# Optimization experiments

Measured on AMD Instinct MI355X. Metric: run time of the kernel, lower is better.

Reference implementation:

```python
import jax, jax.numpy as jnp
import numpy as np


def _conv1x1(x, w, b):
    # x: [B,C,H,W], w: [O,C], b: [O] -> [B,O,H,W]
    return jnp.einsum('bchw,oc->bohw', x, w) + b[None, :, None, None]


def setup_inputs() -> dict:
    key = jax.random.key(0)
    ks = jax.random.split(key, 5)
    B, C, H, W = 4, 256, 64, 64
    C2 = C // 2
    scale = 0.02  # keep attention logits in a sane range
    return {
        'x': jax.random.normal(ks[0], (B, C, H, W), dtype=jnp.float32),
        'w_theta': jax.random.normal(ks[1], (C2, C), dtype=jnp.float32) * scale,
        'b_theta': jnp.zeros((C2,), dtype=jnp.float32),
        'w_phi': jax.random.normal(ks[2], (C2, C), dtype=jnp.float32) * scale,
        'b_phi': jnp.zeros((C2,), dtype=jnp.float32),
        'w_g': jax.random.normal(ks[3], (C2, C), dtype=jnp.float32) * scale,
        'b_g': jnp.zeros((C2,), dtype=jnp.float32),
        'w_out': jax.random.normal(ks[4], (C, C2), dtype=jnp.float32) * scale,
        'b_out': jnp.zeros((C,), dtype=jnp.float32),
    }


def reference(x, w_theta, b_theta, w_phi, b_phi, w_g, b_g, w_out, b_out):
    B, C, H, W = x.shape
    C2 = C // 2
    N = H * W
    theta = _conv1x1(x, w_theta, b_theta).reshape(B, C2, N)  # [B,C2,N]
    phi = _conv1x1(x, w_phi, b_phi).reshape(B, C2, N)        # [B,C2,N]
    g = _conv1x1(x, w_g, b_g).reshape(B, C2, N)              # [B,C2,N]
    # non-local attention: scores[b,m,n] = theta[b,:,m] . phi[b,:,n]
    scores = jnp.einsum('bcm,bcn->bmn', theta, phi)          # [B,N,N]
    attn = jax.nn.softmax(scores, axis=-1)                   # [B,N,N]
    # output = g @ attn^T : out[b,c,m] = sum_n g[b,c,n] * attn[b,m,n]
    out = jnp.einsum('bcn,bmn->bcm', g, attn)                # [B,C2,N]
    out = out.reshape(B, C2, H, W)
    return x + _conv1x1(out, w_out, b_out)
```

## Files before the change

kernel.cpp:

```cpp
#include <hip/hip_runtime.h>
#include <hip/hip_bf16.h>

#define B_  4
#define C_  256
#define C2_ 128
#define N_  4096
#define LOG2E 1.4426950408889634f

typedef unsigned short u16;
typedef __attribute__((ext_vector_type(8))) short bf16x8;
typedef __attribute__((ext_vector_type(4))) float f32x4;

static __device__ __forceinline__ u16 f2bf(float f) {
    return __builtin_bit_cast(u16, __float2bfloat16(f));
}
static __device__ __forceinline__ float bf2f(u16 u) {
    return __bfloat162float(__builtin_bit_cast(__hip_bfloat16, u));
}

__global__ __launch_bounds__(256) void prepw_kernel(
    const float* __restrict__ wt, const float* __restrict__ wp,
    const float* __restrict__ wg, const float* __restrict__ wo,
    u16* __restrict__ Wb) {
    int i = (blockIdx.x * 256 + threadIdx.x) * 4;
    int mat = i >> 15, off = i & 32767;
    const float* src = mat == 0 ? wt : (mat == 1 ? wp : (mat == 2 ? wg : wo));
    float4 v = *(const float4*)(src + off);
    ushort4 o = { f2bf(v.x), f2bf(v.y), f2bf(v.z), f2bf(v.w) };
    *(ushort4*)(Wb + i) = o;
}

__global__ __launch_bounds__(256) void projx_kernel(
    const float* __restrict__ x, const u16* __restrict__ Wb,
    const float* __restrict__ b_theta, const float* __restrict__ b_phi,
    const float* __restrict__ b_g,
    u16* __restrict__ Q, u16* __restrict__ K, u16* __restrict__ V) {
    __shared__ __align__(16) union {
        u16 XTs[32][264];
        u16 Vt[128][40];
    } sm;
    int bid = blockIdx.x;
    int b   = bid / (N_ / 32);
    int n0  = (bid % (N_ / 32)) * 32;
    int tid = threadIdx.x;
    int wave = tid >> 6, lane = tid & 63, quad = lane >> 4, l16 = lane & 15;
    int mgrp = wave >> 1, chalf = wave & 1;

#pragma unroll
    for (int it = 0; it < 4; ++it) {
        int idx = it * 256 + tid;
        int q = idx & 7, p = idx >> 3;
        const float* r0 = x + ((size_t)b * C_ + 2 * p) * N_ + n0 + 4 * q;
        float4 v0 = *(const float4*)r0;
        float4 v1 = *(const float4*)(r0 + N_);
        const float* f0 = (const float*)&v0;
        const float* f1 = (const float*)&v1;
#pragma unroll
        for (int j = 0; j < 4; ++j) {
            unsigned pk = (unsigned)f2bf(f0[j]) | ((unsigned)f2bf(f1[j]) << 16);
            *(unsigned*)&sm.XTs[4 * q + j][2 * p] = pk;
        }
    }
    __syncthreads();

    bf16x8 af[8];
#pragma unroll
    for (int ks = 0; ks < 8; ++ks)
        af[ks] = *(const bf16x8*)&sm.XTs[mgrp * 16 + l16][ks * 32 + quad * 8];
    __syncthreads();

    const float* biases[3] = { b_theta, b_phi, b_g };
#pragma unroll
    for (int mat = 0; mat < 3; ++mat) {
        const u16* wm = Wb + (size_t)mat * C2_ * C_;
        const float* bias = biases[mat];
        f32x4 acc[4];
#pragma unroll
        for (int i = 0; i < 4; ++i) acc[i] = (f32x4){0.f, 0.f, 0.f, 0.f};
#pragma unroll
        for (int ct = 0; ct < 4; ++ct) {
            int ce = chalf * 4 + ct;
            const u16* wr = wm + (size_t)(ce * 16 + l16) * C_ + quad * 8;
#pragma unroll
            for (int ks = 0; ks < 8; ++ks) {
                bf16x8 bf = *(const bf16x8*)(wr + ks * 32);
                acc[ct] = __builtin_amdgcn_mfma_f32_16x16x32_bf16(af[ks], bf, acc[ct], 0, 0, 0);
            }
        }
        if (mat < 2) {
            u16* dst = mat == 0 ? Q : K;
            float sc = mat == 0 ? LOG2E : 1.0f;
#pragma unroll
            for (int ct = 0; ct < 4; ++ct) {
                int c2 = (chalf * 4 + ct) * 16 + l16;
                float bb = bias[c2];
#pragma unroll
                for (int r = 0; r < 4; ++r) {
                    int n = n0 + mgrp * 16 + quad * 4 + r;
                    dst[((size_t)b * N_ + n) * C2_ + c2] = f2bf((acc[ct][r] + bb) * sc);
                }
            }
        } else {
#pragma unroll
            for (int ct = 0; ct < 4; ++ct) {
                int c2 = (chalf * 4 + ct) * 16 + l16;
                float bb = bias[c2];
#pragma unroll
                for (int r = 0; r < 4; ++r)
                    sm.Vt[c2][mgrp * 16 + quad * 4 + r] = f2bf(acc[ct][r] + bb);
            }
        }
    }
    __syncthreads();
    {
        int row = tid >> 1, col16 = (tid & 1) * 16;
        uint4 a0 = *(const uint4*)&sm.Vt[row][col16];
        uint4 a1 = *(const uint4*)&sm.Vt[row][col16 + 8];
        u16* vp = V + ((size_t)b * C2_ + row) * N_ + n0 + col16;
        *(uint4*)vp = a0;
        *(uint4*)(vp + 8) = a1;
    }
}

__global__ __launch_bounds__(256, 2) void attn_kernel(
    const u16* __restrict__ Q, const u16* __restrict__ K,
    const u16* __restrict__ V, u16* __restrict__ AO,
    u16* __restrict__ Opb, float* __restrict__ lsum, int nsplit) {
    const int BM = 128, BN = 64, D = C2_;
    const int per = B_ * (N_ / BM);
    int s    = blockIdx.x / per;
    int r0   = blockIdx.x % per;
    int b    = r0 / (N_ / BM);
    int m0   = (r0 % (N_ / BM)) * BM;
    int tid  = threadIdx.x;
    int wave = tid >> 6, lane = tid & 63, quad = (lane >> 4) & 3, l16 = lane & 15;

    __shared__ __align__(16) u16 Ks[BN][D + 8];
    __shared__ __align__(16) u16 Vs[D][BN + 8];
    __shared__ __align__(16) u16 Psb[4][32][BN + 8];
    u16* Ps = &Psb[wave][0][0];

    bf16x8 qf[2][4];
#pragma unroll
    for (int ms = 0; ms < 2; ++ms) {
        const u16* qp = Q + ((size_t)b * N_ + m0 + wave * 32 + ms * 16 + l16) * D;
#pragma unroll
        for (int kk = 0; kk < 4; ++kk)
            qf[ms][kk] = *(const bf16x8*)(qp + kk * 32 + quad * 8);
    }

    float l_r[2][4] = {{0.f, 0.f, 0.f, 0.f}, {0.f, 0.f, 0.f, 0.f}};
    f32x4 o_acc[2][8];
#pragma unroll
    for (int ms = 0; ms < 2; ++ms)
#pragma unroll
        for (int i = 0; i < 8; ++i) o_acc[ms][i] = (f32x4){0.f, 0.f, 0.f, 0.f};

    const int tiles = N_ / BN;
    const int base = tiles / nsplit, rem = tiles % nsplit;
    const int t0 = s * base + (s < rem ? s : rem);
    const int cnt = base + (s < rem ? 1 : 0);
    const int nt0 = t0 * BN, nt1 = (t0 + cnt) * BN;

    for (int nt = nt0; nt < nt1; nt += BN) {
        const u16* kp = K + ((size_t)b * N_ + nt) * D;
#pragma unroll
        for (int it = 0; it < 4; ++it) {
            int idx = it * 256 + tid;
            int row = idx >> 4, col = (idx & 15) * 8;
            *(uint4*)&Ks[row][col] = *(const uint4*)(kp + row * D + col);
        }
#pragma unroll
        for (int it = 0; it < 4; ++it) {
            int idx = it * 256 + tid;
            int row = idx >> 3, col = (idx & 7) * 8;
            *(uint4*)&Vs[row][col] =
                *(const uint4*)(V + ((size_t)b * C2_ + row) * N_ + nt + col);
        }
        __syncthreads();

        f32x4 sc[2][4];
#pragma unroll
        for (int nn = 0; nn < 4; ++nn) {
            f32x4 a0 = (f32x4){0.f, 0.f, 0.f, 0.f};
            f32x4 a1 = (f32x4){0.f, 0.f, 0.f, 0.f};
#pragma unroll
            for (int kk = 0; kk < 4; ++kk) {
                bf16x8 kf = *(const bf16x8*)&Ks[nn * 16 + l16][kk * 32 + quad * 8];
                a0 = __builtin_amdgcn_mfma_f32_16x16x32_bf16(qf[0][kk], kf, a0, 0, 0, 0);
                a1 = __builtin_amdgcn_mfma_f32_16x16x32_bf16(qf[1][kk], kf, a1, 0, 0, 0);
            }
            sc[0][nn] = a0;
            sc[1][nn] = a1;
        }

#pragma unroll
        for (int ms = 0; ms < 2; ++ms)
#pragma unroll
            for (int nn = 0; nn < 4; ++nn)
#pragma unroll
                for (int r = 0; r < 4; ++r) {
                    float p = __builtin_amdgcn_exp2f(sc[ms][nn][r]);
                    l_r[ms][r] += p;
                    Ps[(ms * 16 + quad * 4 + r) * (BN + 8) + nn * 16 + l16] = f2bf(p);
                }

#pragma unroll
        for (int ks = 0; ks < 2; ++ks) {
            bf16x8 pf0 = *(const bf16x8*)&Ps[(l16) * (BN + 8) + ks * 32 + quad * 8];
            bf16x8 pf1 = *(const bf16x8*)&Ps[(16 + l16) * (BN + 8) + ks * 32 + quad * 8];
#pragma unroll
            for (int cs = 0; cs < 8; ++cs) {
                bf16x8 vf = *(const bf16x8*)&Vs[cs * 16 + l16][ks * 32 + quad * 8];
                o_acc[0][cs] = __builtin_amdgcn_mfma_f32_16x16x32_bf16(pf0, vf, o_acc[0][cs], 0, 0, 0);
                o_acc[1][cs] = __builtin_amdgcn_mfma_f32_16x16x32_bf16(pf1, vf, o_acc[1][cs], 0, 0, 0);
            }
        }
        __syncthreads();
    }

#pragma unroll
    for (int ms = 0; ms < 2; ++ms)
#pragma unroll
        for (int r = 0; r < 4; ++r) {
            l_r[ms][r] += __shfl_xor(l_r[ms][r], 1);
            l_r[ms][r] += __shfl_xor(l_r[ms][r], 2);
            l_r[ms][r] += __shfl_xor(l_r[ms][r], 4);
            l_r[ms][r] += __shfl_xor(l_r[ms][r], 8);
        }

    if (Opb) {
#pragma unroll
        for (int ms = 0; ms < 2; ++ms) {
#pragma unroll
            for (int cs = 0; cs < 8; ++cs)
#pragma unroll
                for (int r = 0; r < 4; ++r) {
                    size_t row = (size_t)s * (B_ * N_) + (size_t)b * N_ +
                                 m0 + wave * 32 + ms * 16 + quad * 4 + r;
                    Opb[row * C2_ + cs * 16 + l16] = f2bf(o_acc[ms][cs][r]);
                }
            if (l16 == 0)
#pragma unroll
                for (int r = 0; r < 4; ++r) {
                    size_t row = (size_t)s * (B_ * N_) + (size_t)b * N_ +
                                 m0 + wave * 32 + ms * 16 + quad * 4 + r;
                    lsum[row] = l_r[ms][r];
                }
        }
    } else {
#pragma unroll
        for (int ms = 0; ms < 2; ++ms)
#pragma unroll
            for (int cs = 0; cs < 8; ++cs)
#pragma unroll
                for (int r = 0; r < 4; ++r) {
                    float v = o_acc[ms][cs][r] / l_r[ms][r];
                    AO[((size_t)b * N_ + m0 + wave * 32 + ms * 16 + quad * 4 + r) * C2_ +
                       cs * 16 + l16] = f2bf(v);
                }
    }
}

__global__ __launch_bounds__(256) void outproj_kernel(
    const float* __restrict__ x, const u16* __restrict__ Opb,
    const float* __restrict__ lsum, const u16* __restrict__ AO,
    const u16* __restrict__ Wob, const float* __restrict__ b_out,
    float* __restrict__ y, int nsplit) {
    __shared__ __align__(16) u16 As[64][C2_ + 8];
    __shared__ float Ls[64];
    int bid = blockIdx.x;
    int per_b = (C_ / 64) * (N_ / 64);
    int b   = bid / per_b;
    int rem = bid % per_b;
    int c0  = (rem / (N_ / 64)) * 64;
    int n0  = (rem % (N_ / 64)) * 64;
    int tid = threadIdx.x;
    int wave = tid >> 6, lane = tid & 63, quad = lane >> 4, l16 = lane & 15;

    if (nsplit > 1) {
        if (tid < 64) {
            float L = 0.f;
            for (int s = 0; s < nsplit; ++s)
                L += lsum[(size_t)s * (B_ * N_) + (size_t)b * N_ + n0 + tid];
            Ls[tid] = 1.f / L;
        }
        __syncthreads();
#pragma unroll
        for (int it = 0; it < 4; ++it) {
            int idx = it * 256 + tid;
            int n = idx >> 4, c8 = (idx & 15) * 8;
            float a[8] = {0.f, 0.f, 0.f, 0.f, 0.f, 0.f, 0.f, 0.f};
            for (int s = 0; s < nsplit; ++s) {
                const u16* op = Opb +
                    ((size_t)s * (B_ * N_) + (size_t)b * N_ + n0 + n) * C2_ + c8;
                uint4 raw = *(const uint4*)op;
                const u16* rp = (const u16*)&raw;
#pragma unroll
                for (int j = 0; j < 8; ++j) a[j] += bf2f(rp[j]);
            }
            float inv = Ls[n];
            u16 o[8];
#pragma unroll
            for (int j = 0; j < 8; ++j) o[j] = f2bf(a[j] * inv);
            *(uint4*)&As[n][c8] = *(const uint4*)o;
        }
    } else {
#pragma unroll
        for (int it = 0; it < 4; ++it) {
            int idx = it * 256 + tid;
            int n = idx >> 4, c8 = (idx & 15) * 8;
            *(uint4*)&As[n][c8] =
                *(const uint4*)(AO + ((size_t)b * N_ + n0 + n) * C2_ + c8);
        }
    }
    __syncthreads();

    int cw = c0 + wave * 16;
    bf16x8 af[4];
#pragma unroll
    for (int kk = 0; kk < 4; ++kk)
        af[kk] = *(const bf16x8*)&Wob[(size_t)(cw + l16) * C2_ + kk * 32 + quad * 8];

    f32x4 acc[4];
#pragma unroll
    for (int i = 0; i < 4; ++i) acc[i] = (f32x4){0.f, 0.f, 0.f, 0.f};

#pragma unroll
    for (int nn = 0; nn < 4; ++nn)
#pragma unroll
        for (int kk = 0; kk < 4; ++kk) {
            bf16x8 bf = *(const bf16x8*)&As[nn * 16 + l16][kk * 32 + quad * 8];
            acc[nn] = __builtin_amdgcn_mfma_f32_16x16x32_bf16(af[kk], bf, acc[nn], 0, 0, 0);
        }

    float bo[4];
#pragma unroll
    for (int r = 0; r < 4; ++r) bo[r] = b_out[cw + quad * 4 + r];

#pragma unroll
    for (int nn = 0; nn < 4; ++nn)
#pragma unroll
        for (int r = 0; r < 4; ++r) {
            int c = cw + quad * 4 + r;
            size_t off = ((size_t)b * C_ + c) * N_ + n0 + nn * 16 + l16;
            y[off] = x[off] + bo[r] + acc[nn][r];
        }
}

extern "C" void kernel_launch(void* const* d_in, const int* in_sizes, int n_in,
                              void* d_out, int out_size, void* d_ws, size_t ws_size,
                              hipStream_t stream) {
    const float* x       = (const float*)d_in[0];
    const float* w_theta = (const float*)d_in[1];
    const float* b_theta = (const float*)d_in[2];
    const float* w_phi   = (const float*)d_in[3];
    const float* b_phi   = (const float*)d_in[4];
    const float* w_g     = (const float*)d_in[5];
    const float* b_g     = (const float*)d_in[6];
    const float* w_out   = (const float*)d_in[7];
    const float* b_out   = (const float*)d_in[8];
    float* y = (float*)d_out;

    const size_t SZ = (size_t)B_ * N_ * C2_;
    u16* Q  = (u16*)d_ws;
    u16* K  = Q + SZ;
    u16* V  = K + SZ;
    u16* AO = V + SZ;
    u16* Wb = AO + SZ;
    u16* Wob = Wb + (size_t)3 * C2_ * C_;
    char* dyn = (char*)(Wb + (size_t)4 * C2_ * C_);
    size_t fixedB = (size_t)(dyn - (char*)d_ws);

    size_t perS = SZ * 2 + (size_t)B_ * N_ * 4;

    int S;
    if      (ws_size >= fixedB + 6 * perS) S = 6;
    else if (ws_size >= fixedB + 4 * perS) S = 4;
    else if (ws_size >= fixedB + 2 * perS) S = 2;
    else                                   S = 1;

    u16*   Opb = nullptr;
    float* ls  = nullptr;
    if (S > 1) {
        Opb = (u16*)dyn;
        ls  = (float*)(Opb + (size_t)S * SZ);
    }

    prepw_kernel<<<128, 256, 0, stream>>>(w_theta, w_phi, w_g, w_out, Wb);
    projx_kernel<<<B_ * (N_ / 32), 256, 0, stream>>>(
        x, Wb, b_theta, b_phi, b_g, Q, K, V);
    attn_kernel<<<B_ * (N_ / 128) * S, 256, 0, stream>>>(Q, K, V, AO, Opb, ls, S);
    outproj_kernel<<<B_ * (C_ / 64) * (N_ / 64), 256, 0, stream>>>(
        x, Opb, ls, AO, Wob, b_out, y, S);
}
```

Measured before the change: 179.8 us.

## Fuse weight bf16 conversion into projection and out-proj kernels; drop prep kernel

Removes the separate weight-prep launch. The projection and output-projection kernels now read fp32 weights, convert them to bf16 and stage them in shared memory. The projection tile grows from 32 to 64 positions, with each wave owning 16 rows and weights loaded in two 64-row halves per matrix. The maximum split count for attention drops from 6 to 4, which changes the attention parallelism and the cost of the merge. The trade is one fewer launch against repeated fp32 weight conversion in every block and extra barriers.

```diff
diff --git a/kernel.cpp b/kernel.cpp
--- a/kernel.cpp
+++ b/kernel.cpp
@@ -17,39 +17,34 @@
 static __device__ __forceinline__ float bf2f(u16 u) {
     return __bfloat162float(__builtin_bit_cast(__hip_bfloat16, u));
 }
-
-__global__ __launch_bounds__(256) void prepw_kernel(
+static __device__ __forceinline__ bf16x8 cvt8(const float* p) {
+    u16 t[8];
+#pragma unroll
+    for (int j = 0; j < 8; ++j) t[j] = f2bf(p[j]);
+    return *(const bf16x8*)t;
+}
+
+__global__ __launch_bounds__(256, 2) void projx_kernel(
+    const float* __restrict__ x,
     const float* __restrict__ wt, const float* __restrict__ wp,
-    const float* __restrict__ wg, const float* __restrict__ wo,
-    u16* __restrict__ Wb) {
-    int i = (blockIdx.x * 256 + threadIdx.x) * 4;
-    int mat = i >> 15, off = i & 32767;
-    const float* src = mat == 0 ? wt : (mat == 1 ? wp : (mat == 2 ? wg : wo));
-    float4 v = *(const float4*)(src + off);
-    ushort4 o = { f2bf(v.x), f2bf(v.y), f2bf(v.z), f2bf(v.w) };
-    *(ushort4*)(Wb + i) = o;
-}
-
-__global__ __launch_bounds__(256) void projx_kernel(
-    const float* __restrict__ x, const u16* __restrict__ Wb,
+    const float* __restrict__ wg,
     const float* __restrict__ b_theta, const float* __restrict__ b_phi,
     const float* __restrict__ b_g,
     u16* __restrict__ Q, u16* __restrict__ K, u16* __restrict__ V) {
-    __shared__ __align__(16) union {
-        u16 XTs[32][264];
-        u16 Vt[128][40];
-    } sm;
+    __shared__ __align__(16) u16 XTs[64][264];
+    __shared__ __align__(16) u16 Ws[64][264];
+    u16 (*Vt)[72] = (u16(*)[72])XTs;
+
     int bid = blockIdx.x;
-    int b   = bid / (N_ / 32);
-    int n0  = (bid % (N_ / 32)) * 32;
+    int b   = bid / (N_ / 64);
+    int n0  = (bid % (N_ / 64)) * 64;
     int tid = threadIdx.x;
-    int wave = tid >> 6, lane = tid & 63, quad = lane >> 4, l16 = lane & 15;
-    int mgrp = wave >> 1, chalf = wave & 1;
-
-#pragma unroll
-    for (int it = 0; it < 4; ++it) {
+    int wave = tid >> 6, lane = tid & 63, quad = (lane >> 4) & 3, l16 = lane & 15;
+
+#pragma unroll
+    for (int it = 0; it < 8; ++it) {
         int idx = it * 256 + tid;
-        int q = idx & 7, p = idx >> 3;
+        int q = idx & 15, p = idx >> 4;
         const float* r0 = x + ((size_t)b * C_ + 2 * p) * N_ + n0 + 4 * q;
         float4 v0 = *(const float4*)r0;
         float4 v1 = *(const float4*)(r0 + N_);
@@ -58,7 +53,7 @@
 #pragma unroll
         for (int j = 0; j < 4; ++j) {
             unsigned pk = (unsigned)f2bf(f0[j]) | ((unsigned)f2bf(f1[j]) << 16);
-            *(unsigned*)&sm.XTs[4 * q + j][2 * p] = pk;
+            *(unsigned*)&XTs[4 * q + j][2 * p] = pk;
         }
     }
     __syncthreads();
@@ -66,59 +61,77 @@
     bf16x8 af[8];
 #pragma unroll
     for (int ks = 0; ks < 8; ++ks)
-        af[ks] = *(const bf16x8*)&sm.XTs[mgrp * 16 + l16][ks * 32 + quad * 8];
+        af[ks] = *(const bf16x8*)&XTs[wave * 16 + l16][ks * 32 + quad * 8];
     __syncthreads();
 
+    const float* wms[3]    = { wt, wp, wg };
     const float* biases[3] = { b_theta, b_phi, b_g };
+
 #pragma unroll
     for (int mat = 0; mat < 3; ++mat) {
-        const u16* wm = Wb + (size_t)mat * C2_ * C_;
+        const float* wm = wms[mat];
         const float* bias = biases[mat];
-        f32x4 acc[4];
-#pragma unroll
-        for (int i = 0; i < 4; ++i) acc[i] = (f32x4){0.f, 0.f, 0.f, 0.f};
-#pragma unroll
-        for (int ct = 0; ct < 4; ++ct) {
-            int ce = chalf * 4 + ct;
-            const u16* wr = wm + (size_t)(ce * 16 + l16) * C_ + quad * 8;
-#pragma unroll
-            for (int ks = 0; ks < 8; ++ks) {
-                bf16x8 bf = *(const bf16x8*)(wr + ks * 32);
-                acc[ct] = __builtin_amdgcn_mfma_f32_16x16x32_bf16(af[ks], bf, acc[ct], 0, 0, 0);
+#pragma unroll
+        for (int h = 0; h < 2; ++h) {
+#pragma unroll
+            for (int it = 0; it < 8; ++it) {
+                int idx = it * 256 + tid;
+                int row = idx >> 5, c8 = (idx & 31) * 8;
+                const float* src = wm + (size_t)(h * 64 + row) * C_ + c8;
+                float w8[8];
+                *(float4*)&w8[0] = *(const float4*)src;
+                *(float4*)&w8[4] = *(const float4*)(src + 4);
+                bf16x8 v = cvt8(w8);
+                *(bf16x8*)&Ws[row][c8] = v;
             }
-        }
-        if (mat < 2) {
-            u16* dst = mat == 0 ? Q : K;
-            float sc = mat == 0 ? LOG2E : 1.0f;
-#pragma unroll
-            for (int ct = 0; ct < 4; ++ct) {
-                int c2 = (chalf * 4 + ct) * 16 + l16;
-                float bb = bias[c2];
-#pragma unroll
-                for (int r = 0; r < 4; ++r) {
-                    int n = n0 + mgrp * 16 + quad * 4 + r;
-                    dst[((size_t)b * N_ + n) * C2_ + c2] = f2bf((acc[ct][r] + bb) * sc);
+            __syncthreads();
+
+            f32x4 acc[4];
+#pragma unroll
+            for (int i = 0; i < 4; ++i) acc[i] = (f32x4){0.f, 0.f, 0.f, 0.f};
+#pragma unroll
+            for (int ct = 0; ct < 4; ++ct)
+#pragma unroll
+                for (int ks = 0; ks < 8; ++ks) {
+                    bf16x8 bf = *(const bf16x8*)&Ws[ct * 16 + l16][ks * 32 + quad * 8];
+                    acc[ct] = __builtin_amdgcn_mfma_f32_16x16x32_bf16(
+                        af[ks], bf, acc[ct], 0, 0, 0);
+                }
+
+            if (mat < 2) {
+                u16* dst = mat == 0 ? Q : K;
+                float sc = mat == 0 ? LOG2E : 1.0f;
+#pragma unroll
+                for (int ct = 0; ct < 4; ++ct) {
+                    int c2 = h * 64 + ct * 16 + l16;
+                    float bb = bias[c2];
+#pragma unroll
+                    for (int r = 0; r < 4; ++r) {
+                        int n = n0 + wave * 16 + quad * 4 + r;
+                        dst[((size_t)b * N_ + n) * C2_ + c2] =
+                            f2bf((acc[ct][r] + bb) * sc);
+                    }
+                }
+            } else {
+#pragma unroll
+                for (int ct = 0; ct < 4; ++ct) {
+                    int c2 = h * 64 + ct * 16 + l16;
+                    float bb = bias[c2];
+#pragma unroll
+                    for (int r = 0; r < 4; ++r)
+                        Vt[c2][wave * 16 + quad * 4 + r] = f2bf(acc[ct][r] + bb);
                 }
             }
-        } else {
-#pragma unroll
-            for (int ct = 0; ct < 4; ++ct) {
-                int c2 = (chalf * 4 + ct) * 16 + l16;
-                float bb = bias[c2];
-#pragma unroll
-                for (int r = 0; r < 4; ++r)
-                    sm.Vt[c2][mgrp * 16 + quad * 4 + r] = f2bf(acc[ct][r] + bb);
-            }
-        }
-    }
-    __syncthreads();
-    {
-        int row = tid >> 1, col16 = (tid & 1) * 16;
-        uint4 a0 = *(const uint4*)&sm.Vt[row][col16];
-        uint4 a1 = *(const uint4*)&sm.Vt[row][col16 + 8];
-        u16* vp = V + ((size_t)b * C2_ + row) * N_ + n0 + col16;
-        *(uint4*)vp = a0;
-        *(uint4*)(vp + 8) = a1;
+            __syncthreads();
+        }
+    }
+
+#pragma unroll
+    for (int it = 0; it < 4; ++it) {
+        int idx = it * 256 + tid;
+        int row = idx >> 3, n8 = (idx & 7) * 8;
+        *(uint4*)(V + ((size_t)b * C2_ + row) * N_ + n0 + n8) =
+            *(const uint4*)&Vt[row][n8];
     }
 }
 
@@ -265,9 +278,10 @@
 __global__ __launch_bounds__(256) void outproj_kernel(
     const float* __restrict__ x, const u16* __restrict__ Opb,
     const float* __restrict__ lsum, const u16* __restrict__ AO,
-    const u16* __restrict__ Wob, const float* __restrict__ b_out,
+    const float* __restrict__ w_out, const float* __restrict__ b_out,
     float* __restrict__ y, int nsplit) {
     __shared__ __align__(16) u16 As[64][C2_ + 8];
+    __shared__ __align__(16) u16 Ws2[64][C2_ + 8];
     __shared__ float Ls[64];
     int bid = blockIdx.x;
     int per_b = (C_ / 64) * (N_ / 64);
@@ -276,7 +290,19 @@
     int c0  = (rem / (N_ / 64)) * 64;
     int n0  = (rem % (N_ / 64)) * 64;
     int tid = threadIdx.x;
-    int wave = tid >> 6, lane = tid & 63, quad = lane >> 4, l16 = lane & 15;
+    int wave = tid >> 6, lane = tid & 63, quad = (lane >> 4) & 3, l16 = lane & 15;
+
+#pragma unroll
+    for (int it = 0; it < 4; ++it) {
+        int idx = it * 256 + tid;
+        int row = idx >> 4, c8 = (idx & 15) * 8;
+        const float* src = w_out + (size_t)(c0 + row) * C2_ + c8;
+        float w8[8];
+        *(float4*)&w8[0] = *(const float4*)src;
+        *(float4*)&w8[4] = *(const float4*)(src + 4);
+        bf16x8 v = cvt8(w8);
+        *(bf16x8*)&Ws2[row][c8] = v;
+    }
 
     if (nsplit > 1) {
         if (tid < 64) {
@@ -316,11 +342,10 @@
     }
     __syncthreads();
 
-    int cw = c0 + wave * 16;
     bf16x8 af[4];
 #pragma unroll
     for (int kk = 0; kk < 4; ++kk)
-        af[kk] = *(const bf16x8*)&Wob[(size_t)(cw + l16) * C2_ + kk * 32 + quad * 8];
+        af[kk] = *(const bf16x8*)&Ws2[wave * 16 + l16][kk * 32 + quad * 8];
 
     f32x4 acc[4];
 #pragma unroll
@@ -334,6 +359,7 @@
             acc[nn] = __builtin_amdgcn_mfma_f32_16x16x32_bf16(af[kk], bf, acc[nn], 0, 0, 0);
         }
 
+    int cw = c0 + wave * 16;
     float bo[4];
 #pragma unroll
     for (int r = 0; r < 4; ++r) bo[r] = b_out[cw + quad * 4 + r];
@@ -363,23 +389,20 @@
     float* y = (float*)d_out;
 
     const size_t SZ = (size_t)B_ * N_ * C2_;
-    u16* Q  = (u16*)d_ws;
-    u16* K  = Q + SZ;
-    u16* V  = K + SZ;
-    u16* AO = V + SZ;
-    u16* Wb = AO + SZ;
-    u16* Wob = Wb + (size_t)3 * C2_ * C_;
-    char* dyn = (char*)(Wb + (size_t)4 * C2_ * C_);
-    size_t fixedB = (size_t)(dyn - (char*)d_ws);
+    u16* Q = (u16*)d_ws;
+    u16* K = Q + SZ;
+    u16* V = K + SZ;
+    char* dyn = (char*)(V + SZ);
+    size_t fixedB = 3 * SZ * 2;
 
     size_t perS = SZ * 2 + (size_t)B_ * N_ * 4;
 
     int S;
-    if      (ws_size >= fixedB + 6 * perS) S = 6;
-    else if (ws_size >= fixedB + 4 * perS) S = 4;
+    if      (ws_size >= fixedB + 4 * perS) S = 4;
     else if (ws_size >= fixedB + 2 * perS) S = 2;
     else                                   S = 1;
 
+    u16*   AO  = (u16*)dyn;
     u16*   Opb = nullptr;
     float* ls  = nullptr;
     if (S > 1) {
@@ -387,10 +410,9 @@
         ls  = (float*)(Opb + (size_t)S * SZ);
     }
 
-    prepw_kernel<<<128, 256, 0, stream>>>(w_theta, w_phi, w_g, w_out, Wb);
-    projx_kernel<<<B_ * (N_ / 32), 256, 0, stream>>>(
-        x, Wb, b_theta, b_phi, b_g, Q, K, V);
+    projx_kernel<<<B_ * (N_ / 64), 256, 0, stream>>>(
+        x, w_theta, w_phi, w_g, b_theta, b_phi, b_g, Q, K, V);
     attn_kernel<<<B_ * (N_ / 128) * S, 256, 0, stream>>>(Q, K, V, AO, Opb, ls, S);
     outproj_kernel<<<B_ * (C_ / 64) * (N_ / 64), 256, 0, stream>>>(
-        x, Opb, ls, AO, Wob, b_out, y, S);
-}
+        x, Opb, ls, AO, w_out, b_out, y, S);
+}
```

Result: faster. 155.7 us, median of 2 (-13.4%).
